# Performance work log

Hardware: AMD Instinct MI355X
Metric: run time of the kernel (lower is better)

The kernel has to match this reference:

```python
import jax, jax.numpy as jnp
import numpy as np
from jax import lax

PAD = (3, 3)
PAD_VALUE = -1.0
POOL_SIZE = 7
POOL_STRIDE = 2


def setup_inputs() -> dict:
    key = jax.random.key(0)
    k1, k2 = jax.random.split(key)
    B, Cin, L = 64, 64, 16384
    Cout, K = 128, 7
    I = jax.random.normal(k1, (B, Cin, L), dtype=jnp.float32)
    W = jax.random.normal(k2, (Cout, Cin, K), dtype=jnp.float32)
    # Threshold params are initialized to ones in the module (requires_grad=False)
    threshold_plus = jnp.ones((Cout,), dtype=jnp.float32)
    threshold_minus = jnp.ones((Cout,), dtype=jnp.float32)
    threshold_plus_sign = jnp.ones((Cout,), dtype=jnp.float32)
    threshold_minus_sign = jnp.ones((Cout,), dtype=jnp.float32)
    return {
        "I": I,
        "W": W,
        "threshold_plus": threshold_plus,
        "threshold_minus": threshold_minus,
        "threshold_plus_sign": threshold_plus_sign,
        "threshold_minus_sign": threshold_minus_sign,
    }


def reference(I, W, threshold_plus, threshold_minus, threshold_plus_sign, threshold_minus_sign):
    # 1) ConstantPad1d(padding=(3,3), value=-1.0)
    x = jnp.pad(I, ((0, 0), (0, 0), PAD), constant_values=PAD_VALUE)
    # 2) Binarize activations and weights via sign(), then float conv1d (no bias)
    ba = jnp.sign(x)
    bw = jnp.sign(W)
    conv = lax.conv_general_dilated(
        ba, bw,
        window_strides=(1,),
        padding="VALID",
        dimension_numbers=("NCH", "OIH", "NCH"),
    )  # [B, Cout, L]
    # 3) MaxPool1d(kernel_size=7, stride=2)
    pooled = lax.reduce_window(
        conv, -jnp.inf, lax.max,
        window_dimensions=(1, 1, POOL_SIZE),
        window_strides=(1, 1, POOL_STRIDE),
        padding="VALID",
    )  # [B, Cout, Lp]
    # 4) Per-channel Threshold (vectorized over channels; 2*c > 2*t == c > t)
    tp = threshold_plus[None, :, None]
    tm = threshold_minus[None, :, None]
    ps = threshold_plus_sign[None, :, None]
    ms = threshold_minus_sign[None, :, None]
    pos_branch = jnp.where(pooled > tp, ps, -ps)
    neg_branch = jnp.where(pooled > tm, ms, -ms)
    out = jnp.where(pooled >= 0, pos_branch, neg_branch)
    return out
```

## Files before the change

### kernel.cpp

```cpp
#include <hip/hip_runtime.h>
#include <stdint.h>

#define B_    64
#define CIN   64
#define L_IN  16384
#define COUT  128
#define K_    7
#define LPAD  3
#define LP    (L_IN + 2*LPAD)
#define LPA   16416
#define LOUT  8189
#define NTERMS 448
#define TOUT  8
#define CO_PER_BLK 16

__global__ __launch_bounds__(256) void pack_A(const float* __restrict__ I,
                                              uint64_t* __restrict__ A) {
    int b     = blockIdx.x >> 4;
    int chunk = blockIdx.x & 15;
    int t     = threadIdx.x;
    int l0    = chunk * 1024 + t * 4;
    const uint32_t* Ib = (const uint32_t*)(I + (size_t)b * CIN * L_IN + l0);
    uint32_t lo0 = 0, lo1 = 0, lo2 = 0, lo3 = 0;
    uint32_t hi0 = 0, hi1 = 0, hi2 = 0, hi3 = 0;
#pragma unroll 8
    for (int ci = 0; ci < 32; ++ci) {
        uint4 v = *(const uint4*)(Ib + (size_t)ci * L_IN);
        lo0 |= (v.x >> 31) << ci;
        lo1 |= (v.y >> 31) << ci;
        lo2 |= (v.z >> 31) << ci;
        lo3 |= (v.w >> 31) << ci;
    }
#pragma unroll 8
    for (int ci = 0; ci < 32; ++ci) {
        uint4 v = *(const uint4*)(Ib + (size_t)(ci + 32) * L_IN);
        hi0 |= (v.x >> 31) << ci;
        hi1 |= (v.y >> 31) << ci;
        hi2 |= (v.z >> 31) << ci;
        hi3 |= (v.w >> 31) << ci;
    }
    uint64_t* Ab = A + (size_t)b * LPA + (LPAD + l0);
    Ab[0] = ((uint64_t)hi0 << 32) | lo0;
    Ab[1] = ((uint64_t)hi1 << 32) | lo1;
    Ab[2] = ((uint64_t)hi2 << 32) | lo2;
    Ab[3] = ((uint64_t)hi3 << 32) | lo3;
    if (chunk == 0 && t < 6) {
        int l = (t < 3) ? t : (L_IN + t);
        A[(size_t)b * LPA + l] = ~0ULL;
    }
}

__global__ __launch_bounds__(256) void pack_W(const float* __restrict__ W,
                                              uint64_t* __restrict__ Bp) {
    int idx = blockIdx.x * 256 + threadIdx.x;
    if (idx >= COUT * K_) return;
    int co = idx / K_, k = idx - co * K_;
    uint64_t acc = 0;
#pragma unroll
    for (int ci = 0; ci < CIN; ++ci) {
        uint32_t s = __float_as_uint(W[(size_t)co * CIN * K_ + ci * K_ + k]) >> 31;
        acc |= (uint64_t)s << ci;
    }
    Bp[idx] = acc;
}

__global__ __launch_bounds__(256, 4) void bconv_pool_thresh(
    const uint64_t* __restrict__ A, const uint64_t* __restrict__ Bp,
    const float* __restrict__ tp_, const float* __restrict__ tm_,
    const float* __restrict__ ps_, const float* __restrict__ ms_,
    float* __restrict__ out)
{
    const int cg = blockIdx.x;
    const int lc = blockIdx.y;
    const int b  = blockIdx.z;
    const int t  = threadIdx.x;
    int out0 = lc * 2048 + t * TOUT;
    if (out0 > LOUT - TOUT) out0 = LOUT - TOUT;

    const uint64_t* Ab = A + (size_t)b * LPA + 2 * out0;
    uint64_t a[2 * TOUT + 11];
#pragma unroll
    for (int j = 0; j < 2 * TOUT + 11; ++j) a[j] = Ab[j];

#pragma unroll 1
    for (int ci_ = 0; ci_ < CO_PER_BLK; ++ci_) {
        const int co = cg * CO_PER_BLK + ci_;
        const uint64_t* Bco = Bp + co * K_;
        const uint64_t w0 = Bco[0], w1 = Bco[1], w2 = Bco[2], w3 = Bco[3],
                       w4 = Bco[4], w5 = Bco[5], w6 = Bco[6];

        int s[2 * TOUT + 5];
#pragma unroll
        for (int j = 0; j < 2 * TOUT + 5; ++j) {
            int acc;
            acc  = __popcll(a[j + 0] ^ w0);
            acc += __popcll(a[j + 1] ^ w1);
            acc += __popcll(a[j + 2] ^ w2);
            acc += __popcll(a[j + 3] ^ w3);
            acc += __popcll(a[j + 4] ^ w4);
            acc += __popcll(a[j + 5] ^ w5);
            acc += __popcll(a[j + 6] ^ w6);
            s[j] = acc;
        }

        int p[TOUT + 2];
#pragma unroll
        for (int i = 0; i < TOUT + 2; ++i) p[i] = min(s[2 * i], s[2 * i + 1]);

        const float ftp = (448.0f - tp_[co]) * 0.5f;
        const float ftm = (448.0f - tm_[co]) * 0.5f;
        const float ps = ps_[co], ms = ms_[co];
        float* op = out + ((size_t)(b * COUT + co)) * LOUT + out0;
#pragma unroll
        for (int o = 0; o < TOUT; ++o) {
            int smin = min(min(p[o], p[o + 1]), min(p[o + 2], s[2 * o + 6]));
            float sf  = (float)smin;
            float pos = sf < ftp ? ps : -ps;
            float neg = sf < ftm ? ms : -ms;
            op[o] = (sf <= 224.0f) ? pos : neg;
        }
    }
}

extern "C" void kernel_launch(void* const* d_in, const int* in_sizes, int n_in,
                              void* d_out, int out_size, void* d_ws, size_t ws_size,
                              hipStream_t stream) {
    const float* I  = (const float*)d_in[0];
    const float* W  = (const float*)d_in[1];
    const float* tp = (const float*)d_in[2];
    const float* tm = (const float*)d_in[3];
    const float* ps = (const float*)d_in[4];
    const float* ms = (const float*)d_in[5];
    float* out = (float*)d_out;

    uint64_t* A  = (uint64_t*)d_ws;
    uint64_t* Bp = (uint64_t*)((char*)d_ws + (size_t)B_ * LPA * sizeof(uint64_t));

    hipLaunchKernelGGL(pack_A, dim3(B_ * 16), dim3(256), 0, stream, I, A);
    hipLaunchKernelGGL(pack_W, dim3((COUT * K_ + 255) / 256), dim3(256), 0, stream, W, Bp);
    hipLaunchKernelGGL(bconv_pool_thresh, dim3(8, 4, B_), dim3(256), 0, stream,
                       A, Bp, tp, tm, ps, ms, out);
}
```

Measured before the change: 598.5 us.

## Fuse activation bit-packing into conv kernel via LDS-staged packed window

Drops the separate pack_A kernel and its global workspace round-trip. Each block now packs the sign bits of a 1024-column slice of the input (plus halo) straight into shared memory, using a padded layout to avoid bank conflicts. Its four waves then each handle 32 output channels from that shared window. This removes a kernel launch and the global write/read of the packed activations. In exchange, each block re-reads a small halo, there is an extra barrier, and far fewer blocks are launched (16x64), which may lower parallelism and latency hiding.

After: 602.1 us. About the same (+0.6%).

```diff
diff --git a/kernel.cpp b/kernel.cpp
--- a/kernel.cpp
+++ b/kernel.cpp
@@ -6,49 +6,13 @@
 #define L_IN  16384
 #define COUT  128
 #define K_    7
-#define LPAD  3
-#define LP    (L_IN + 2*LPAD)
-#define LPA   16416
+#define LP    16390
 #define LOUT  8189
-#define NTERMS 448
 #define TOUT  8
-#define CO_PER_BLK 16
-
-__global__ __launch_bounds__(256) void pack_A(const float* __restrict__ I,
-                                              uint64_t* __restrict__ A) {
-    int b     = blockIdx.x >> 4;
-    int chunk = blockIdx.x & 15;
-    int t     = threadIdx.x;
-    int l0    = chunk * 1024 + t * 4;
-    const uint32_t* Ib = (const uint32_t*)(I + (size_t)b * CIN * L_IN + l0);
-    uint32_t lo0 = 0, lo1 = 0, lo2 = 0, lo3 = 0;
-    uint32_t hi0 = 0, hi1 = 0, hi2 = 0, hi3 = 0;
-#pragma unroll 8
-    for (int ci = 0; ci < 32; ++ci) {
-        uint4 v = *(const uint4*)(Ib + (size_t)ci * L_IN);
-        lo0 |= (v.x >> 31) << ci;
-        lo1 |= (v.y >> 31) << ci;
-        lo2 |= (v.z >> 31) << ci;
-        lo3 |= (v.w >> 31) << ci;
-    }
-#pragma unroll 8
-    for (int ci = 0; ci < 32; ++ci) {
-        uint4 v = *(const uint4*)(Ib + (size_t)(ci + 32) * L_IN);
-        hi0 |= (v.x >> 31) << ci;
-        hi1 |= (v.y >> 31) << ci;
-        hi2 |= (v.z >> 31) << ci;
-        hi3 |= (v.w >> 31) << ci;
-    }
-    uint64_t* Ab = A + (size_t)b * LPA + (LPAD + l0);
-    Ab[0] = ((uint64_t)hi0 << 32) | lo0;
-    Ab[1] = ((uint64_t)hi1 << 32) | lo1;
-    Ab[2] = ((uint64_t)hi2 << 32) | lo2;
-    Ab[3] = ((uint64_t)hi3 << 32) | lo3;
-    if (chunk == 0 && t < 6) {
-        int l = (t < 3) ? t : (L_IN + t);
-        A[(size_t)b * LPA + l] = ~0ULL;
-    }
-}
+#define XCHUNK 16
+#define PBLK  512
+#define WBLK  1036
+#define NSLOT 1104
 
 __global__ __launch_bounds__(256) void pack_W(const float* __restrict__ W,
                                               uint64_t* __restrict__ Bp) {
@@ -64,30 +28,76 @@
     Bp[idx] = acc;
 }
 
-__global__ __launch_bounds__(256, 4) void bconv_pool_thresh(
-    const uint64_t* __restrict__ A, const uint64_t* __restrict__ Bp,
+__global__ __launch_bounds__(256, 4) void fused_bconv(
+    const float* __restrict__ I, const uint64_t* __restrict__ Bp,
     const float* __restrict__ tp_, const float* __restrict__ tm_,
     const float* __restrict__ ps_, const float* __restrict__ ms_,
     float* __restrict__ out)
 {
-    const int cg = blockIdx.x;
-    const int lc = blockIdx.y;
-    const int b  = blockIdx.z;
-    const int t  = threadIdx.x;
-    int out0 = lc * 2048 + t * TOUT;
-    if (out0 > LOUT - TOUT) out0 = LOUT - TOUT;
+    __shared__ uint64_t lds[NSLOT];
+    const int x = blockIdx.x;
+    const int b = blockIdx.y;
+    const int t = threadIdx.x;
 
-    const uint64_t* Ab = A + (size_t)b * LPA + 2 * out0;
-    uint64_t a[2 * TOUT + 11];
+    const int colbase = (x << 10) - 4;
+#pragma unroll 1
+    for (int i = 0; i < 2; ++i) {
+        int g = t + (i << 8);
+        if (g < 260) {
+            int col0 = colbase + (g << 2);
+            uint32_t l0 = 0, l1 = 0, l2 = 0, l3 = 0;
+            uint32_t h0 = 0, h1 = 0, h2 = 0, h3 = 0;
+            if ((unsigned)col0 <= (unsigned)(L_IN - 4)) {
+                const uint32_t* Ib = (const uint32_t*)(I + (size_t)b * CIN * L_IN + col0);
+#pragma unroll 8
+                for (int ci = 0; ci < 32; ++ci) {
+                    uint4 v = *(const uint4*)(Ib + (size_t)ci * L_IN);
+                    l0 |= (v.x >> 31) << ci;
+                    l1 |= (v.y >> 31) << ci;
+                    l2 |= (v.z >> 31) << ci;
+                    l3 |= (v.w >> 31) << ci;
+                }
+#pragma unroll 8
+                for (int ci = 0; ci < 32; ++ci) {
+                    uint4 v = *(const uint4*)(Ib + (size_t)(ci + 32) * L_IN);
+                    h0 |= (v.x >> 31) << ci;
+                    h1 |= (v.y >> 31) << ci;
+                    h2 |= (v.z >> 31) << ci;
+                    h3 |= (v.w >> 31) << ci;
+                }
+            }
+            uint64_t w[4] = { ((uint64_t)h0 << 32) | l0, ((uint64_t)h1 << 32) | l1,
+                              ((uint64_t)h2 << 32) | l2, ((uint64_t)h3 << 32) | l3 };
 #pragma unroll
-    for (int j = 0; j < 2 * TOUT + 11; ++j) a[j] = Ab[j];
+            for (int q = 0; q < 4; ++q) {
+                int wl = (g << 2) - 1 + q;
+                if ((unsigned)wl < (unsigned)WBLK) {
+                    int wg = (x << 10) + wl;
+                    uint64_t val = (wg < 3 || wg >= L_IN + 3) ? ~0ULL : w[q];
+                    lds[wl + (wl >> 4)] = val;
+                }
+            }
+        }
+    }
+    __syncthreads();
+
+    const int cs = __builtin_amdgcn_readfirstlane(t >> 6);
+    const int lt = t & 63;
+    const int out0 = x * PBLK + lt * TOUT;
+    const uint64_t* awin = &lds[lt * 17];
+
+    const bool tail = (out0 + TOUT > LOUT);
 
 #pragma unroll 1
-    for (int ci_ = 0; ci_ < CO_PER_BLK; ++ci_) {
-        const int co = cg * CO_PER_BLK + ci_;
+    for (int ci_ = 0; ci_ < 32; ++ci_) {
+        const int co = cs * 32 + ci_;
         const uint64_t* Bco = Bp + co * K_;
         const uint64_t w0 = Bco[0], w1 = Bco[1], w2 = Bco[2], w3 = Bco[3],
                        w4 = Bco[4], w5 = Bco[5], w6 = Bco[6];
+
+        uint64_t a[27];
+#pragma unroll
+        for (int m = 0; m < 27; ++m) a[m] = awin[m + (m >> 4)];
 
         int s[2 * TOUT + 5];
 #pragma unroll
@@ -111,13 +121,23 @@
         const float ftm = (448.0f - tm_[co]) * 0.5f;
         const float ps = ps_[co], ms = ms_[co];
         float* op = out + ((size_t)(b * COUT + co)) * LOUT + out0;
+
+        float r[TOUT];
 #pragma unroll
         for (int o = 0; o < TOUT; ++o) {
             int smin = min(min(p[o], p[o + 1]), min(p[o + 2], s[2 * o + 6]));
             float sf  = (float)smin;
             float pos = sf < ftp ? ps : -ps;
             float neg = sf < ftm ? ms : -ms;
-            op[o] = (sf <= 224.0f) ? pos : neg;
+            r[o] = (sf <= 224.0f) ? pos : neg;
+        }
+        if (!tail) {
+#pragma unroll
+            for (int o = 0; o < TOUT; ++o) op[o] = r[o];
+        } else {
+#pragma unroll
+            for (int o = 0; o < TOUT; ++o)
+                if (out0 + o < LOUT) op[o] = r[o];
         }
     }
 }
@@ -133,11 +153,9 @@
     const float* ms = (const float*)d_in[5];
     float* out = (float*)d_out;
 
-    uint64_t* A  = (uint64_t*)d_ws;
-    uint64_t* Bp = (uint64_t*)((char*)d_ws + (size_t)B_ * LPA * sizeof(uint64_t));
+    uint64_t* Bp = (uint64_t*)d_ws;
 
-    hipLaunchKernelGGL(pack_A, dim3(B_ * 16), dim3(256), 0, stream, I, A);
     hipLaunchKernelGGL(pack_W, dim3((COUT * K_ + 255) / 256), dim3(256), 0, stream, W, Bp);
-    hipLaunchKernelGGL(bconv_pool_thresh, dim3(8, 4, B_), dim3(256), 0, stream,
-                       A, Bp, tp, tm, ps, ms, out);
+    hipLaunchKernelGGL(fused_bconv, dim3(XCHUNK, B_), dim3(256), 0, stream,
+                       I, Bp, tp, tm, ps, ms, out);
 }
```
